# Kernel tuning notes

Hardware: AMD Instinct MI355X
Metric: run time of the kernel (lower is better)

Reference implementation:

```python
import jax, jax.numpy as jnp
import numpy as np

N_NODES = 100000


def _graph_conv(x, W, b, src, dst, n_nodes):
    # dgl GraphConv, norm='both'. in_dim >= out_dim so weight is applied first.
    E = src.shape[0]
    ones = jnp.ones((E,), dtype=x.dtype)
    deg_out = jnp.clip(jax.ops.segment_sum(ones, src, num_segments=n_nodes), 1.0)
    deg_in = jnp.clip(jax.ops.segment_sum(ones, dst, num_segments=n_nodes), 1.0)
    h = x @ W                                  # [N, out]
    h = h * (deg_out ** -0.5)[:, None]          # src-side norm D_out^{-1/2}
    agg = jax.ops.segment_sum(h[src], dst, num_segments=n_nodes)  # SpMM
    agg = agg * (deg_in ** -0.5)[:, None]       # dst-side norm D_in^{-1/2}
    return agg + b


def setup_inputs() -> dict:
    key = jax.random.key(0)
    k1, k2, k3, k4, k5, k6, k7 = jax.random.split(key, 7)
    in_dim, hidden_dim, out_dim = 256, 128, 40
    E = 3200000
    h = jax.random.normal(k1, (N_NODES, in_dim), dtype=jnp.float32)
    src = jax.random.randint(k2, (E,), 0, N_NODES)
    dst = jax.random.randint(k3, (E,), 0, N_NODES)
    # Glorot-style init for GraphConv weights, zero bias (dgl default)
    W1 = jax.random.normal(k4, (in_dim, hidden_dim), dtype=jnp.float32) / np.sqrt(in_dim)
    b1 = jnp.zeros((hidden_dim,), dtype=jnp.float32)
    W2 = jax.random.normal(k5, (hidden_dim, out_dim), dtype=jnp.float32) / np.sqrt(hidden_dim)
    b2 = jnp.zeros((out_dim,), dtype=jnp.float32)
    return {"h": h, "W1": W1, "b1": b1, "W2": W2, "b2": b2, "src": src, "dst": dst}


def reference(h, W1, b1, W2, b2, src, dst):
    n = h.shape[0]
    # CRD: GraphConv -> relu (dropout is identity in eval)
    x = _graph_conv(h, W1, b1, src, dst, n)
    x = jax.nn.relu(x)
    # CLS: GraphConv -> log_softmax over classes
    x = _graph_conv(x, W2, b2, src, dst, n)
    return jax.nn.log_softmax(x, axis=1)
```

## Files before the change

kernel.cpp:

```cpp
#include <hip/hip_runtime.h>
#include <hip/hip_bf16.h>
#include <cstddef>
#include <cstdint>

#define IN_DIM 256
#define HID 128
#define OUT_DIM 40

#define CHUNK 4096
#define BIN_SHIFT 10
#define BIN_SIZE 1024
#define MAXB 128
#define GSPLIT 8

typedef __attribute__((ext_vector_type(8))) short short8;
typedef __attribute__((ext_vector_type(4))) float f32x4;
typedef __attribute__((ext_vector_type(2))) float f32x2;

__device__ inline short f2bf(float f) {
    __hip_bfloat16 b = __float2bfloat16(f);
    return __builtin_bit_cast(short, b);
}
__device__ inline float bf2f(unsigned short u) {
    unsigned int v = (unsigned int)u << 16;
    return __builtin_bit_cast(float, v);
}
__device__ inline int permf(int p) { return (p >> 3) + 16 * (p & 7); }

__global__ __launch_bounds__(256) void k_init(const float* __restrict__ W1, const float* __restrict__ W2,
                                              const float* __restrict__ b1, short* __restrict__ Wg,
                                              short* __restrict__ Wg2, float* __restrict__ b1p,
                                              int* __restrict__ deg_in, int* __restrict__ deg_out, int Z,
                                              const int* __restrict__ src, const int* __restrict__ dst,
                                              uint32_t* __restrict__ stD, unsigned short* __restrict__ stS,
                                              int* __restrict__ bboD, int* __restrict__ bboS,
                                              int E, int NBINS, int setupBlocks) {
    __shared__ __align__(16) uint32_t sgD[CHUNK];
    __shared__ __align__(16) unsigned short sgS[CHUNK];
    __shared__ int hD[MAXB], hS[MAXB], sd[MAXB];
    int t = threadIdx.x;
    if (blockIdx.x < setupBlocks) {
        int flat = blockIdx.x * 256 + t;
        if (flat < 8192) {
            int k = flat >> 5;
            int n0 = (flat & 31) * 4;
            float4 v = *(const float4*)(W1 + (size_t)k * HID + n0);
            int ks = k >> 5, quad = (k >> 3) & 3, j = k & 7;
            float vv[4] = {v.x, v.y, v.z, v.w};
#pragma unroll
            for (int e = 0; e < 4; ++e) {
                int n = n0 + e;
                int nt = n >> 4;
                int ln = (n & 15) | (quad << 4);
                Wg[(((nt * 8 + ks) * 64) + ln) * 8 + j] = f2bf(vv[e]);
            }
            return;
        }
        flat -= 8192;
        if (flat < 3 * 4 * 64 * 8) {
            int f = flat >> 9;
            int ln = (flat >> 3) & 63;
            int j = flat & 7;
            int nt = f >> 2, ks = f & 3;
            int q = ks * 32 + (ln >> 4) * 8 + j;
            int c = nt * 16 + (ln & 15);
            float v = (c < OUT_DIM) ? W2[(size_t)permf(q) * OUT_DIM + c] : 0.f;
            Wg2[flat] = f2bf(v);
            return;
        }
        flat -= 3 * 4 * 64 * 8;
        if (flat < HID) { b1p[flat] = b1[permf(flat)]; return; }
        flat -= HID;
        if (flat < Z) { *(int4*)(deg_in + flat * 4) = make_int4(0, 0, 0, 0); return; }
        flat -= Z;
        if (flat < Z) { *(int4*)(deg_out + flat * 4) = make_int4(0, 0, 0, 0); }
        return;
    }
    int j = blockIdx.x - setupBlocks;
    int base = j * CHUNK;
    int nE = min(CHUNK, E - base);
    int NB1 = NBINS + 1;
    for (int i = t; i < MAXB; i += 256) { hD[i] = 0; hS[i] = 0; }
    __syncthreads();
    for (int i = t; i < nE; i += 256) {
        atomicAdd(&hD[dst[base + i] >> BIN_SHIFT], 1);
        atomicAdd(&hS[src[base + i] >> BIN_SHIFT], 1);
    }
    __syncthreads();
    if (t < MAXB) sd[t] = hD[t];
    __syncthreads();
    for (int off = 1; off < MAXB; off <<= 1) {
        int x = 0;
        if (t < MAXB && t >= off) x = sd[t - off];
        __syncthreads();
        if (t < MAXB) sd[t] += x;
        __syncthreads();
    }
    if (t < MAXB) {
        int h = hD[t];
        int c = sd[t] - h;
        hD[t] = c;
        if (t < NBINS) bboD[(size_t)j * NB1 + t] = c;
    }
    if (t == NBINS) bboD[(size_t)j * NB1 + NBINS] = nE;
    __syncthreads();
    if (t < MAXB) sd[t] = hS[t];
    __syncthreads();
    for (int off = 1; off < MAXB; off <<= 1) {
        int x = 0;
        if (t < MAXB && t >= off) x = sd[t - off];
        __syncthreads();
        if (t < MAXB) sd[t] += x;
        __syncthreads();
    }
    if (t < MAXB) {
        int h = hS[t];
        int c = sd[t] - h;
        hS[t] = c;
        if (t < NBINS) bboS[(size_t)j * NB1 + t] = c;
    }
    if (t == NBINS) bboS[(size_t)j * NB1 + NBINS] = nE;
    __syncthreads();
    for (int i = t; i < nE; i += 256) {
        int s = src[base + i], d = dst[base + i];
        int pD = atomicAdd(&hD[d >> BIN_SHIFT], 1);
        sgD[pD] = ((uint32_t)(d & (BIN_SIZE - 1)) << 17) | (uint32_t)s;
        int pS = atomicAdd(&hS[s >> BIN_SHIFT], 1);
        sgS[pS] = (unsigned short)(s & (BIN_SIZE - 1));
    }
    __syncthreads();
    int nh = nE >> 1;
    uint2* dD = (uint2*)(stD + base);
    const uint2* sD = (const uint2*)sgD;
    for (int i = t; i < nh; i += 256) dD[i] = sD[i];
    uint32_t* dS = (uint32_t*)(stS + base);
    const uint32_t* sS = (const uint32_t*)sgS;
    for (int i = t; i < nh; i += 256) dS[i] = sS[i];
    if ((nE & 1) && t == 0) { stD[base + nE - 1] = sgD[nE - 1]; stS[base + nE - 1] = sgS[nE - 1]; }
}

__global__ __launch_bounds__(256) void k_deg(const uint32_t* __restrict__ stD, const int* __restrict__ bboD,
                                             const unsigned short* __restrict__ stS, const int* __restrict__ bboS,
                                             int* __restrict__ deg_in, int* __restrict__ deg_out,
                                             int* __restrict__ hsave, int nchunk, int NBINS) {
    __shared__ int hist[BIN_SIZE];
    int b = blockIdx.x, g = blockIdx.y, t = threadIdx.x;
    int wv = t >> 6, lane = t & 63;
    int NB1 = NBINS + 1;
    for (int i = t; i < BIN_SIZE; i += 256) hist[i] = 0;
    __syncthreads();
    int base = b << BIN_SHIFT;
    if (blockIdx.z == 0) {
        for (int j = g * 4 + wv; j < nchunk; j += GSPLIT * 4) {
            int s = bboD[(size_t)j * NB1 + b], e = bboD[(size_t)j * NB1 + b + 1];
            const uint32_t* seg = stD + (size_t)j * CHUNK;
            for (int i = s + lane; i < e; i += 64)
                atomicAdd(&hist[seg[i] >> 17], 1);
        }
        __syncthreads();
        int* hp = hsave + ((size_t)(b * GSPLIT + g) << BIN_SHIFT);
        for (int i = t; i < BIN_SIZE; i += 256) {
            int v = hist[i];
            hp[i] = v;
            if (v) atomicAdd(&deg_in[base + i], v);
        }
    } else {
        for (int j = g * 4 + wv; j < nchunk; j += GSPLIT * 4) {
            int s = bboS[(size_t)j * NB1 + b], e = bboS[(size_t)j * NB1 + b + 1];
            const unsigned short* seg = stS + (size_t)j * CHUNK;
            for (int i = s + lane; i < e; i += 64)
                atomicAdd(&hist[seg[i]], 1);
        }
        __syncthreads();
        for (int i = t; i < BIN_SIZE; i += 256) {
            int v = hist[i];
            if (v) atomicAdd(&deg_out[base + i], v);
        }
    }
}

__global__ __launch_bounds__(256) void k_scan1(const int* __restrict__ deg, int* __restrict__ out,
                                               int* __restrict__ bsum, float* __restrict__ rs_in, int n) {
    __shared__ int sd[256];
    int t = threadIdx.x, b = blockIdx.x;
    int base = b * 1024 + t * 4;
    int v0 = 0, v1 = 0, v2 = 0, v3 = 0;
    if (base + 0 < n) v0 = deg[base + 0];
    if (base + 1 < n) v1 = deg[base + 1];
    if (base + 2 < n) v2 = deg[base + 2];
    if (base + 3 < n) v3 = deg[base + 3];
    if (base + 0 < n) rs_in[base + 0] = rsqrtf((float)max(v0, 1));
    if (base + 1 < n) rs_in[base + 1] = rsqrtf((float)max(v1, 1));
    if (base + 2 < n) rs_in[base + 2] = rsqrtf((float)max(v2, 1));
    if (base + 3 < n) rs_in[base + 3] = rsqrtf((float)max(v3, 1));
    int ts = v0 + v1 + v2 + v3;
    sd[t] = ts;
    __syncthreads();
    for (int off = 1; off < 256; off <<= 1) {
        int x = 0;
        if (t >= off) x = sd[t - off];
        __syncthreads();
        sd[t] += x;
        __syncthreads();
    }
    int excl = sd[t] - ts;
    if (base + 0 < n) out[base + 0] = excl;
    if (base + 1 < n) out[base + 1] = excl + v0;
    if (base + 2 < n) out[base + 2] = excl + v0 + v1;
    if (base + 3 < n) out[base + 3] = excl + v0 + v1 + v2;
    if (t == 255) bsum[b] = sd[255];
}

__global__ __launch_bounds__(256) void k_scan3(int* __restrict__ row_ptr, const int* __restrict__ bsum,
                                               int* __restrict__ cursor, const int* __restrict__ deg_out,
                                               float* __restrict__ rs_out, int n, int E, int NB) {
    __shared__ int sb[128];
    int t = threadIdx.x;
    if (t < 128) sb[t] = (t < NB) ? bsum[t] : 0;
    __syncthreads();
    for (int off = 1; off < 128; off <<= 1) {
        int x = 0;
        if (t < 128 && t >= off) x = sb[t - off];
        __syncthreads();
        if (t < 128) sb[t] += x;
        __syncthreads();
    }
    int i = blockIdx.x * 256 + threadIdx.x;
    if (i < n) {
        int blk = i >> 10;
        int add = (blk > 0) ? sb[blk - 1] : 0;
        int v = row_ptr[i] + add;
        row_ptr[i] = v;
        cursor[i] = v;
        rs_out[i] = rsqrtf((float)max(deg_out[i], 1));
    }
    if (i == 0) row_ptr[n] = E;
}

__global__ __launch_bounds__(256) void k_colgemm1(const uint32_t* __restrict__ stD, const int* __restrict__ bboD,
                                                  const int* __restrict__ hsave, int* __restrict__ cursor,
                                                  int* __restrict__ col, int nchunk, int NBINS, int colBlocks,
                                                  const float* __restrict__ A, const short* __restrict__ Wg,
                                                  const float* __restrict__ rs_out, uint32_t* __restrict__ h1f,
                                                  int M) {
    __shared__ int hist[BIN_SIZE];
    int t = threadIdx.x;
    if (blockIdx.x < colBlocks) {
        int b = blockIdx.x / GSPLIT, g = blockIdx.x % GSPLIT;
        int wv = t >> 6, lane = t & 63;
        int NB1 = NBINS + 1;
        int base = b << BIN_SHIFT;
        const int* hp = hsave + ((size_t)(b * GSPLIT + g) << BIN_SHIFT);
        for (int i = t; i < BIN_SIZE; i += 256) {
            int v = hp[i];
            hist[i] = v ? atomicAdd(&cursor[base + i], v) : 0;
        }
        __syncthreads();
        for (int j = g * 4 + wv; j < nchunk; j += GSPLIT * 4) {
            int s = bboD[(size_t)j * NB1 + b], e = bboD[(size_t)j * NB1 + b + 1];
            const uint32_t* seg = stD + (size_t)j * CHUNK;
            for (int i = s + lane; i < e; i += 64) {
                uint32_t v = seg[i];
                int pos = atomicAdd(&hist[v >> 17], 1);
                col[pos] = (int)(v & 0x1FFFFu);
            }
        }
        return;
    }
    int lane = t & 63, wv = t >> 6;
    int block_row = (blockIdx.x - colBlocks) * 64;
    int row = block_row + wv * 16 + (lane & 15);
    bool valid = row < M;
    const float* ap = A + (size_t)row * IN_DIM + (lane >> 4) * 8;
    f32x4 acc[8] = {};
#pragma unroll
    for (int ks = 0; ks < 8; ++ks) {
        float4 va = {0.f, 0.f, 0.f, 0.f}, vb = {0.f, 0.f, 0.f, 0.f};
        if (valid) {
            va = *(const float4*)(ap + ks * 32);
            vb = *(const float4*)(ap + ks * 32 + 4);
        }
        short8 a;
        a[0] = f2bf(va.x); a[1] = f2bf(va.y); a[2] = f2bf(va.z); a[3] = f2bf(va.w);
        a[4] = f2bf(vb.x); a[5] = f2bf(vb.y); a[6] = f2bf(vb.z); a[7] = f2bf(vb.w);
#pragma unroll
        for (int nt = 0; nt < 8; ++nt) {
            short8 b = *(const short8*)&Wg[(((nt * 8 + ks) * 64) + lane) * 8];
            acc[nt] = __builtin_amdgcn_mfma_f32_16x16x32_bf16(a, b, acc[nt], 0, 0, 0);
        }
    }
    int quad = lane >> 4, cl = lane & 15;
#pragma unroll
    for (int r = 0; r < 4; ++r) {
        int gr = block_row + wv * 16 + quad * 4 + r;
        if (gr >= M) continue;
        float sc = rs_out[gr];
        int d0 = __builtin_amdgcn_cvt_pk_fp8_f32(acc[0][r] * sc, acc[1][r] * sc, 0, false);
        d0 = __builtin_amdgcn_cvt_pk_fp8_f32(acc[2][r] * sc, acc[3][r] * sc, d0, true);
        int d1 = __builtin_amdgcn_cvt_pk_fp8_f32(acc[4][r] * sc, acc[5][r] * sc, 0, false);
        d1 = __builtin_amdgcn_cvt_pk_fp8_f32(acc[6][r] * sc, acc[7][r] * sc, d1, true);
        uint2 dd = make_uint2((uint32_t)d0, (uint32_t)d1);
        *(uint2*)((char*)h1f + (size_t)gr * 128 + cl * 8) = dd;
    }
}

__global__ __launch_bounds__(256) void k_spmm1f(const char* __restrict__ h1c, const int* __restrict__ rp,
                                                const int* __restrict__ col, const float* __restrict__ rs_in,
                                                const float* __restrict__ rs_out, const float* __restrict__ b1p,
                                                const short* __restrict__ Wg2,
                                                uint32_t* __restrict__ h2f, int N) {
    __shared__ uint32_t x1s[16 * 64];
    __shared__ uint32_t hs2[48];
    int t = threadIdx.x;
    int wv = t >> 6, lane = t & 63;
    int grp = lane >> 4, ql = lane & 15;
    int w_base = blockIdx.x * 4;
    int w = w_base + wv;

    float4 blo = *(const float4*)&b1p[ql * 8];
    float4 bhi = *(const float4*)&b1p[ql * 8 + 4];

    if (w < N) {
        int s = rp[w], e = rp[w + 1];
        f32x2 a0 = {0.f, 0.f}, a1 = {0.f, 0.f}, a2 = {0.f, 0.f}, a3 = {0.f, 0.f};
        int qoff = ql << 3;
        int i = s;
        while (i < e) {
            int cnt = min(64, e - i);
            int cl = (lane < cnt) ? lane : cnt - 1;
            int rof = col[i + cl] << 7;
            int nfull = cnt & ~15;
            int it = 0;
            for (; it < nfull; it += 16) {
                int o0 = __shfl(rof, it + grp, 64) + qoff;
                int o1 = __shfl(rof, it + 4 + grp, 64) + qoff;
                int o2 = __shfl(rof, it + 8 + grp, 64) + qoff;
                int o3 = __shfl(rof, it + 12 + grp, 64) + qoff;
                uint2 u0 = *(const uint2*)(h1c + (uint32_t)o0);
                uint2 u1 = *(const uint2*)(h1c + (uint32_t)o1);
                uint2 u2 = *(const uint2*)(h1c + (uint32_t)o2);
                uint2 u3 = *(const uint2*)(h1c + (uint32_t)o3);
                a0 += __builtin_amdgcn_cvt_pk_f32_fp8(u0.x, false);
                a1 += __builtin_amdgcn_cvt_pk_f32_fp8(u0.x, true);
                a2 += __builtin_amdgcn_cvt_pk_f32_fp8(u0.y, false);
                a3 += __builtin_amdgcn_cvt_pk_f32_fp8(u0.y, true);
                a0 += __builtin_amdgcn_cvt_pk_f32_fp8(u1.x, false);
                a1 += __builtin_amdgcn_cvt_pk_f32_fp8(u1.x, true);
                a2 += __builtin_amdgcn_cvt_pk_f32_fp8(u1.y, false);
                a3 += __builtin_amdgcn_cvt_pk_f32_fp8(u1.y, true);
                a0 += __builtin_amdgcn_cvt_pk_f32_fp8(u2.x, false);
                a1 += __builtin_amdgcn_cvt_pk_f32_fp8(u2.x, true);
                a2 += __builtin_amdgcn_cvt_pk_f32_fp8(u2.y, false);
                a3 += __builtin_amdgcn_cvt_pk_f32_fp8(u2.y, true);
                a0 += __builtin_amdgcn_cvt_pk_f32_fp8(u3.x, false);
                a1 += __builtin_amdgcn_cvt_pk_f32_fp8(u3.x, true);
                a2 += __builtin_amdgcn_cvt_pk_f32_fp8(u3.y, false);
                a3 += __builtin_amdgcn_cvt_pk_f32_fp8(u3.y, true);
            }
            if (it < cnt) {
                int e0 = it + grp;
                int o0 = __shfl(rof, e0, 64) + qoff;
                int o1 = __shfl(rof, e0 + 4, 64) + qoff;
                int o2 = __shfl(rof, e0 + 8, 64) + qoff;
                int o3 = __shfl(rof, e0 + 12, 64) + qoff;
                float mv0 = (e0 < cnt) ? 1.f : 0.f;
                float mv1 = (e0 + 4 < cnt) ? 1.f : 0.f;
                float mv2 = (e0 + 8 < cnt) ? 1.f : 0.f;
                float mv3 = (e0 + 12 < cnt) ? 1.f : 0.f;
                f32x2 m0 = {mv0, mv0}, m1 = {mv1, mv1}, m2 = {mv2, mv2}, m3 = {mv3, mv3};
                uint2 u0 = *(const uint2*)(h1c + (uint32_t)o0);
                uint2 u1 = *(const uint2*)(h1c + (uint32_t)o1);
                uint2 u2 = *(const uint2*)(h1c + (uint32_t)o2);
                uint2 u3 = *(const uint2*)(h1c + (uint32_t)o3);
                a0 += __builtin_amdgcn_cvt_pk_f32_fp8(u0.x, false) * m0;
                a1 += __builtin_amdgcn_cvt_pk_f32_fp8(u0.x, true) * m0;
                a2 += __builtin_amdgcn_cvt_pk_f32_fp8(u0.y, false) * m0;
                a3 += __builtin_amdgcn_cvt_pk_f32_fp8(u0.y, true) * m0;
                a0 += __builtin_amdgcn_cvt_pk_f32_fp8(u1.x, false) * m1;
                a1 += __builtin_amdgcn_cvt_pk_f32_fp8(u1.x, true) * m1;
                a2 += __builtin_amdgcn_cvt_pk_f32_fp8(u1.y, false) * m1;
                a3 += __builtin_amdgcn_cvt_pk_f32_fp8(u1.y, true) * m1;
                a0 += __builtin_amdgcn_cvt_pk_f32_fp8(u2.x, false) * m2;
                a1 += __builtin_amdgcn_cvt_pk_f32_fp8(u2.x, true) * m2;
                a2 += __builtin_amdgcn_cvt_pk_f32_fp8(u2.y, false) * m2;
                a3 += __builtin_amdgcn_cvt_pk_f32_fp8(u2.y, true) * m2;
                a0 += __builtin_amdgcn_cvt_pk_f32_fp8(u3.x, false) * m3;
                a1 += __builtin_amdgcn_cvt_pk_f32_fp8(u3.x, true) * m3;
                a2 += __builtin_amdgcn_cvt_pk_f32_fp8(u3.y, false) * m3;
                a3 += __builtin_amdgcn_cvt_pk_f32_fp8(u3.y, true) * m3;
            }
            i += cnt;
        }
        float ac[8] = {a0.x, a0.y, a1.x, a1.y, a2.x, a2.y, a3.x, a3.y};
#pragma unroll
        for (int j = 0; j < 8; ++j) {
            ac[j] += __shfl_xor(ac[j], 16, 64);
            ac[j] += __shfl_xor(ac[j], 32, 64);
        }
        if (lane < 16) {
            float sc = rs_in[w];
            float f0, f1;
            uint32_t o0, o1, o2, o3;
            f0 = fmaxf(fmaf(ac[0], sc, blo.x), 0.f); f1 = fmaxf(fmaf(ac[1], sc, blo.y), 0.f);
            o0 = (uint32_t)(unsigned short)f2bf(f0) | ((uint32_t)(unsigned short)f2bf(f1) << 16);
            f0 = fmaxf(fmaf(ac[2], sc, blo.z), 0.f); f1 = fmaxf(fmaf(ac[3], sc, blo.w), 0.f);
            o1 = (uint32_t)(unsigned short)f2bf(f0) | ((uint32_t)(unsigned short)f2bf(f1) << 16);
            f0 = fmaxf(fmaf(ac[4], sc, bhi.x), 0.f); f1 = fmaxf(fmaf(ac[5], sc, bhi.y), 0.f);
            o2 = (uint32_t)(unsigned short)f2bf(f0) | ((uint32_t)(unsigned short)f2bf(f1) << 16);
            f0 = fmaxf(fmaf(ac[6], sc, bhi.z), 0.f); f1 = fmaxf(fmaf(ac[7], sc, bhi.w), 0.f);
            o3 = (uint32_t)(unsigned short)f2bf(f0) | ((uint32_t)(unsigned short)f2bf(f1) << 16);
            int woff = (wv * 256 + ql * 16) ^ ((wv & 7) << 4);
            *(uint4*)((char*)x1s + woff) = make_uint4(o0, o1, o2, o3);
        }
    }
    __syncthreads();
    int vr = min(4, N - w_base);
    if (wv < 3) {
        short8 wf0 = *(const short8*)&Wg2[((wv * 4 + 0) * 64 + lane) * 8];
        short8 wf1 = *(const short8*)&Wg2[((wv * 4 + 1) * 64 + lane) * 8];
        short8 wf2 = *(const short8*)&Wg2[((wv * 4 + 2) * 64 + lane) * 8];
        short8 wf3 = *(const short8*)&Wg2[((wv * 4 + 3) * 64 + lane) * 8];
        int row = lane & 15, kc = lane >> 4;
        int rbase = row * 256 + kc * 16;
        int swz = (row & 7) << 4;
        f32x4 c = {};
        c = __builtin_amdgcn_mfma_f32_16x16x32_bf16(*(short8*)((char*)x1s + ((rbase + 0) ^ swz)),   wf0, c, 0, 0, 0);
        c = __builtin_amdgcn_mfma_f32_16x16x32_bf16(*(short8*)((char*)x1s + ((rbase + 64) ^ swz)),  wf1, c, 0, 0, 0);
        c = __builtin_amdgcn_mfma_f32_16x16x32_bf16(*(short8*)((char*)x1s + ((rbase + 128) ^ swz)), wf2, c, 0, 0, 0);
        c = __builtin_amdgcn_mfma_f32_16x16x32_bf16(*(short8*)((char*)x1s + ((rbase + 192) ^ swz)), wf3, c, 0, 0, 0);
        int cc = wv * 16 + row;
        if (cc < OUT_DIM && kc == 0) {
            float s0 = rs_out[w_base + 0];
            float s1 = (vr > 1) ? rs_out[w_base + 1] : 0.f;
            float s2 = (vr > 2) ? rs_out[w_base + 2] : 0.f;
            float s3 = (vr > 3) ? rs_out[w_base + 3] : 0.f;
            int pk = __builtin_amdgcn_cvt_pk_fp8_f32(c[0] * s0, c[1] * s1, 0, false);
            pk = __builtin_amdgcn_cvt_pk_fp8_f32(c[2] * s2, c[3] * s3, pk, true);
            hs2[cc] = (uint32_t)pk;
        }
    }
    __syncthreads();
    if (t < 64) {
        int node = t >> 4, d = t & 15;
        uint32_t v = 0;
        if (d < 10) {
            int sh = node * 8;
            uint32_t b0 = (hs2[4 * d + 0] >> sh) & 0xffu;
            uint32_t b1 = (hs2[4 * d + 1] >> sh) & 0xffu;
            uint32_t b2 = (hs2[4 * d + 2] >> sh) & 0xffu;
            uint32_t b3 = (hs2[4 * d + 3] >> sh) & 0xffu;
            v = b0 | (b1 << 8) | (b2 << 16) | (b3 << 24);
        }
        if (node < vr) h2f[(size_t)(w_base + node) * 16 + d] = v;
    }
}

__global__ __launch_bounds__(256) void k_spmm2(const char* __restrict__ h2c, const int* __restrict__ rp,
                                               const int* __restrict__ col, const float* __restrict__ rs_in,
                                               const float* __restrict__ b2, float* __restrict__ out, int n) {
    int w = (blockIdx.x * 256 + threadIdx.x) >> 6;
    int lane = threadIdx.x & 63;
    if (w >= n) return;
    int grp = lane >> 3, fl = lane & 7;
    int qoff = fl << 3;
    int s = rp[w], e = rp[w + 1];
    f32x2 a0 = {0.f, 0.f}, a1 = {0.f, 0.f}, a2 = {0.f, 0.f}, a3 = {0.f, 0.f};
    int i = s;
    while (i < e) {
        int cnt = min(64, e - i);
        int cl = (lane < cnt) ? lane : cnt - 1;
        int rof = col[i + cl] << 6;
        int nfull = cnt & ~31;
        int it = 0;
        for (; it < nfull; it += 32) {
            int o0 = __shfl(rof, it + grp, 64) + qoff;
            int o1 = __shfl(rof, it + 8 + grp, 64) + qoff;
            int o2 = __shfl(rof, it + 16 + grp, 64) + qoff;
            int o3 = __shfl(rof, it + 24 + grp, 64) + qoff;
            uint2 u0 = *(const uint2*)(h2c + (uint32_t)o0);
            uint2 u1 = *(const uint2*)(h2c + (uint32_t)o1);
            uint2 u2 = *(const uint2*)(h2c + (uint32_t)o2);
            uint2 u3 = *(const uint2*)(h2c + (uint32_t)o3);
            a0 += __builtin_amdgcn_cvt_pk_f32_fp8(u0.x, false);
            a1 += __builtin_amdgcn_cvt_pk_f32_fp8(u0.x, true);
            a2 += __builtin_amdgcn_cvt_pk_f32_fp8(u0.y, false);
            a3 += __builtin_amdgcn_cvt_pk_f32_fp8(u0.y, true);
            a0 += __builtin_amdgcn_cvt_pk_f32_fp8(u1.x, false);
            a1 += __builtin_amdgcn_cvt_pk_f32_fp8(u1.x, true);
            a2 += __builtin_amdgcn_cvt_pk_f32_fp8(u1.y, false);
            a3 += __builtin_amdgcn_cvt_pk_f32_fp8(u1.y, true);
            a0 += __builtin_amdgcn_cvt_pk_f32_fp8(u2.x, false);
            a1 += __builtin_amdgcn_cvt_pk_f32_fp8(u2.x, true);
            a2 += __builtin_amdgcn_cvt_pk_f32_fp8(u2.y, false);
            a3 += __builtin_amdgcn_cvt_pk_f32_fp8(u2.y, true);
            a0 += __builtin_amdgcn_cvt_pk_f32_fp8(u3.x, false);
            a1 += __builtin_amdgcn_cvt_pk_f32_fp8(u3.x, true);
            a2 += __builtin_amdgcn_cvt_pk_f32_fp8(u3.y, false);
            a3 += __builtin_amdgcn_cvt_pk_f32_fp8(u3.y, true);
        }
        if (it < cnt) {
            int e0 = it + grp;
            int o0 = __shfl(rof, e0, 64) + qoff;
            int o1 = __shfl(rof, e0 + 8, 64) + qoff;
            int o2 = __shfl(rof, e0 + 16, 64) + qoff;
            int o3 = __shfl(rof, e0 + 24, 64) + qoff;
            float mv0 = (e0 < cnt) ? 1.f : 0.f;
            float mv1 = (e0 + 8 < cnt) ? 1.f : 0.f;
            float mv2 = (e0 + 16 < cnt) ? 1.f : 0.f;
            float mv3 = (e0 + 24 < cnt) ? 1.f : 0.f;
            f32x2 m0 = {mv0, mv0}, m1 = {mv1, mv1}, m2 = {mv2, mv2}, m3 = {mv3, mv3};
            uint2 u0 = *(const uint2*)(h2c + (uint32_t)o0);
            uint2 u1 = *(const uint2*)(h2c + (uint32_t)o1);
            uint2 u2 = *(const uint2*)(h2c + (uint32_t)o2);
            uint2 u3 = *(const uint2*)(h2c + (uint32_t)o3);
            a0 += __builtin_amdgcn_cvt_pk_f32_fp8(u0.x, false) * m0;
            a1 += __builtin_amdgcn_cvt_pk_f32_fp8(u0.x, true) * m0;
            a2 += __builtin_amdgcn_cvt_pk_f32_fp8(u0.y, false) * m0;
            a3 += __builtin_amdgcn_cvt_pk_f32_fp8(u0.y, true) * m0;
            a0 += __builtin_amdgcn_cvt_pk_f32_fp8(u1.x, false) * m1;
            a1 += __builtin_amdgcn_cvt_pk_f32_fp8(u1.x, true) * m1;
            a2 += __builtin_amdgcn_cvt_pk_f32_fp8(u1.y, false) * m1;
            a3 += __builtin_amdgcn_cvt_pk_f32_fp8(u1.y, true) * m1;
            a0 += __builtin_amdgcn_cvt_pk_f32_fp8(u2.x, false) * m2;
            a1 += __builtin_amdgcn_cvt_pk_f32_fp8(u2.x, true) * m2;
            a2 += __builtin_amdgcn_cvt_pk_f32_fp8(u2.y, false) * m2;
            a3 += __builtin_amdgcn_cvt_pk_f32_fp8(u2.y, true) * m2;
            a0 += __builtin_amdgcn_cvt_pk_f32_fp8(u3.x, false) * m3;
            a1 += __builtin_amdgcn_cvt_pk_f32_fp8(u3.x, true) * m3;
            a2 += __builtin_amdgcn_cvt_pk_f32_fp8(u3.y, false) * m3;
            a3 += __builtin_amdgcn_cvt_pk_f32_fp8(u3.y, true) * m3;
        }
        i += cnt;
    }
    float ac[8] = {a0.x, a0.y, a1.x, a1.y, a2.x, a2.y, a3.x, a3.y};
#pragma unroll
    for (int j = 0; j < 8; ++j) {
        ac[j] += __shfl_xor(ac[j], 8, 64);
        ac[j] += __shfl_xor(ac[j], 16, 64);
        ac[j] += __shfl_xor(ac[j], 32, 64);
    }
    bool act = lane < 5;
    float sc = rs_in[w];
    int bb = (fl < 5) ? fl * 8 : 0;
    float val[8];
#pragma unroll
    for (int j = 0; j < 8; ++j)
        val[j] = fmaf(ac[j], sc, b2[bb + j]);
    float pm = -INFINITY;
    if (act) {
        pm = val[0];
#pragma unroll
        for (int j = 1; j < 8; ++j) pm = fmaxf(pm, val[j]);
    }
    pm = fmaxf(pm, __shfl_xor(pm, 4, 8));
    pm = fmaxf(pm, __shfl_xor(pm, 2, 8));
    pm = fmaxf(pm, __shfl_xor(pm, 1, 8));
    float ex = 0.f;
    if (act) {
#pragma unroll
        for (int j = 0; j < 8; ++j) ex += expf(val[j] - pm);
    }
    ex += __shfl_xor(ex, 4, 8);
    ex += __shfl_xor(ex, 2, 8);
    ex += __shfl_xor(ex, 1, 8);
    if (act) {
        float l = pm + logf(ex);
        float4 o0 = {val[0] - l, val[1] - l, val[2] - l, val[3] - l};
        float4 o1 = {val[4] - l, val[5] - l, val[6] - l, val[7] - l};
        float* op = out + (size_t)w * OUT_DIM + lane * 8;
        *(float4*)op = o0;
        *(float4*)(op + 4) = o1;
    }
}


extern "C" void kernel_launch(void* const* d_in, const int* in_sizes, int n_in,
                              void* d_out, int out_size, void* d_ws, size_t ws_size,
                              hipStream_t stream) {
    const int N = in_sizes[0] / IN_DIM;
    const int E = in_sizes[5];
    const float* h  = (const float*)d_in[0];
    const float* W1 = (const float*)d_in[1];
    const float* b1 = (const float*)d_in[2];
    const float* W2 = (const float*)d_in[3];
    const float* b2 = (const float*)d_in[4];
    const int* src  = (const int*)d_in[5];
    const int* dst  = (const int*)d_in[6];
    float* out = (float*)d_out;

    const int NBINS  = (N + BIN_SIZE - 1) >> BIN_SHIFT;
    const int NCHUNK = (E + CHUNK - 1) / CHUNK;

    char* w = (char*)d_ws;
    size_t off = 0;
    auto alloc = [&](size_t bytes) -> void* {
        void* p = w + off;
        off += (bytes + 255) & ~(size_t)255;
        return p;
    };
    int* deg_in   = (int*)alloc((size_t)N * 4);
    int* deg_out  = (int*)alloc((size_t)N * 4);
    int* row_ptr  = (int*)alloc((size_t)(N + 1) * 4);
    int* cursor   = (int*)alloc((size_t)N * 4);
    int* bsum     = (int*)alloc(1024 * 4);
    float* rs_out = (float*)alloc((size_t)N * 4);
    float* rs_in  = (float*)alloc((size_t)N * 4);
    int* col      = (int*)alloc((size_t)E * 4);
    int* bboD     = (int*)alloc((size_t)NCHUNK * (NBINS + 1) * 4);
    int* bboS     = (int*)alloc((size_t)NCHUNK * (NBINS + 1) * 4);
    short* Wg     = (short*)alloc((size_t)8 * 8 * 64 * 8 * 2);
    short* Wg2    = (short*)alloc((size_t)3 * 4 * 64 * 8 * 2);
    float* b1p    = (float*)alloc((size_t)HID * 4);
    int* hsave    = (int*)alloc((size_t)NBINS * GSPLIT * BIN_SIZE * 4);
    uint32_t* stD = (uint32_t*)alloc((size_t)E * 4);
    unsigned short* stS = (unsigned short*)alloc((size_t)E * 2);
    uint32_t* h1f = (uint32_t*)alloc((size_t)N * HID);
    uint32_t* h2f = (uint32_t*)alloc((size_t)N * 64);

    int gN = (N + 255) / 256;
    int NB = (N + 1023) / 1024;
    int Z = (N + 3) / 4;
    int setup_units = 8192 + 3 * 4 * 64 * 8 + HID + 2 * Z;
    int setupBlocks = (setup_units + 255) / 256;
    int colBlocks = NBINS * GSPLIT;

    k_init<<<setupBlocks + NCHUNK, 256, 0, stream>>>(W1, W2, b1, Wg, Wg2, b1p, deg_in, deg_out, Z,
                                                     src, dst, stD, stS, bboD, bboS, E, NBINS, setupBlocks);
    k_deg<<<dim3(NBINS, GSPLIT, 2), 256, 0, stream>>>(stD, bboD, stS, bboS, deg_in, deg_out, hsave, NCHUNK, NBINS);
    k_scan1<<<NB, 256, 0, stream>>>(deg_in, row_ptr, bsum, rs_in, N);
    k_scan3<<<gN, 256, 0, stream>>>(row_ptr, bsum, cursor, deg_out, rs_out, N, E, NB);
    k_colgemm1<<<colBlocks + (N + 63) / 64, 256, 0, stream>>>(stD, bboD, hsave, cursor, col, NCHUNK, NBINS,
                                                              colBlocks, h, Wg, rs_out, h1f, N);
    k_spmm1f<<<(N + 3) / 4, 256, 0, stream>>>((const char*)h1f, row_ptr, col, rs_in, rs_out, b1p, Wg2, h2f, N);
    k_spmm2<<<(N + 3) / 4, 256, 0, stream>>>((const char*)h2f, row_ptr, col, rs_in, b2, out, N);
}
```

Before: 416.4 us.

## Scatter CSR columns with one block per bin, dropping per-split histogram save

The column-scatter phase now uses a single block per 1024-node bin that seeds its shared-memory cursors straight from row_ptr. This removes the hsave per-split histogram buffer, the global cursor array and the global atomics that reserved offsets per split. The chunk loop also batches four chunks' bounds and first loads before the atomics to expose memory-level parallelism. In exchange, only about 98 blocks do the scatter instead of roughly 784, so each block serially walks every chunk. That may leave the scatter starved of parallelism unless it overlaps well with the GEMM blocks in the same launch.

After: 459.9 us. +10.5%, slower.

```diff
diff --git a/kernel.cpp b/kernel.cpp
--- a/kernel.cpp
+++ b/kernel.cpp
@@ -142,7 +142,7 @@
 __global__ __launch_bounds__(256) void k_deg(const uint32_t* __restrict__ stD, const int* __restrict__ bboD,
                                              const unsigned short* __restrict__ stS, const int* __restrict__ bboS,
                                              int* __restrict__ deg_in, int* __restrict__ deg_out,
-                                             int* __restrict__ hsave, int nchunk, int NBINS) {
+                                             int nchunk, int NBINS) {
     __shared__ int hist[BIN_SIZE];
     int b = blockIdx.x, g = blockIdx.y, t = threadIdx.x;
     int wv = t >> 6, lane = t & 63;
@@ -158,10 +158,8 @@
                 atomicAdd(&hist[seg[i] >> 17], 1);
         }
         __syncthreads();
-        int* hp = hsave + ((size_t)(b * GSPLIT + g) << BIN_SHIFT);
         for (int i = t; i < BIN_SIZE; i += 256) {
             int v = hist[i];
-            hp[i] = v;
             if (v) atomicAdd(&deg_in[base + i], v);
         }
     } else {
@@ -212,7 +210,7 @@
 }
 
 __global__ __launch_bounds__(256) void k_scan3(int* __restrict__ row_ptr, const int* __restrict__ bsum,
-                                               int* __restrict__ cursor, const int* __restrict__ deg_out,
+                                               const int* __restrict__ deg_out,
                                                float* __restrict__ rs_out, int n, int E, int NB) {
     __shared__ int sb[128];
     int t = threadIdx.x;
@@ -229,46 +227,66 @@
     if (i < n) {
         int blk = i >> 10;
         int add = (blk > 0) ? sb[blk - 1] : 0;
-        int v = row_ptr[i] + add;
-        row_ptr[i] = v;
-        cursor[i] = v;
+        row_ptr[i] += add;
         rs_out[i] = rsqrtf((float)max(deg_out[i], 1));
     }
     if (i == 0) row_ptr[n] = E;
 }
 
 __global__ __launch_bounds__(256) void k_colgemm1(const uint32_t* __restrict__ stD, const int* __restrict__ bboD,
-                                                  const int* __restrict__ hsave, int* __restrict__ cursor,
-                                                  int* __restrict__ col, int nchunk, int NBINS, int colBlocks,
+                                                  const int* __restrict__ row_ptr, int* __restrict__ col,
+                                                  int nchunk, int NBINS,
                                                   const float* __restrict__ A, const short* __restrict__ Wg,
                                                   const float* __restrict__ rs_out, uint32_t* __restrict__ h1f,
                                                   int M) {
-    __shared__ int hist[BIN_SIZE];
+    __shared__ int cur[BIN_SIZE];
     int t = threadIdx.x;
-    if (blockIdx.x < colBlocks) {
-        int b = blockIdx.x / GSPLIT, g = blockIdx.x % GSPLIT;
+    if (blockIdx.x < (unsigned)NBINS) {
+        int b = blockIdx.x;
         int wv = t >> 6, lane = t & 63;
         int NB1 = NBINS + 1;
         int base = b << BIN_SHIFT;
-        const int* hp = hsave + ((size_t)(b * GSPLIT + g) << BIN_SHIFT);
         for (int i = t; i < BIN_SIZE; i += 256) {
-            int v = hp[i];
-            hist[i] = v ? atomicAdd(&cursor[base + i], v) : 0;
-        }
-        __syncthreads();
-        for (int j = g * 4 + wv; j < nchunk; j += GSPLIT * 4) {
-            int s = bboD[(size_t)j * NB1 + b], e = bboD[(size_t)j * NB1 + b + 1];
-            const uint32_t* seg = stD + (size_t)j * CHUNK;
-            for (int i = s + lane; i < e; i += 64) {
-                uint32_t v = seg[i];
-                int pos = atomicAdd(&hist[v >> 17], 1);
-                col[pos] = (int)(v & 0x1FFFFu);
+            int gn = base + i;
+            cur[i] = (gn < M) ? row_ptr[gn] : 0;
+        }
+        __syncthreads();
+        for (int jj = wv * 4; jj < nchunk; jj += 16) {
+            int s[4], e[4];
+            uint32_t v[4];
+            bool av[4];
+#pragma unroll
+            for (int q = 0; q < 4; ++q) {
+                int j = jj + q;
+                bool jv = j < nchunk;
+                s[q] = jv ? bboD[(size_t)j * NB1 + b] : 0;
+                e[q] = jv ? bboD[(size_t)j * NB1 + b + 1] : 0;
             }
+#pragma unroll
+            for (int q = 0; q < 4; ++q) {
+                av[q] = s[q] + lane < e[q];
+                v[q] = av[q] ? stD[(size_t)(jj + q) * CHUNK + s[q] + lane] : 0u;
+            }
+#pragma unroll
+            for (int q = 0; q < 4; ++q) {
+                if (av[q]) {
+                    int pos = atomicAdd(&cur[v[q] >> 17], 1);
+                    col[pos] = (int)(v[q] & 0x1FFFFu);
+                }
+            }
+#pragma unroll
+            for (int q = 0; q < 4; ++q) {
+                for (int i = s[q] + lane + 64; i < e[q]; i += 64) {
+                    uint32_t vv = stD[(size_t)(jj + q) * CHUNK + i];
+                    int pos = atomicAdd(&cur[vv >> 17], 1);
+                    col[pos] = (int)(vv & 0x1FFFFu);
+                }
+            }
         }
         return;
     }
     int lane = t & 63, wv = t >> 6;
-    int block_row = (blockIdx.x - colBlocks) * 64;
+    int block_row = (blockIdx.x - NBINS) * 64;
     int row = block_row + wv * 16 + (lane & 15);
     bool valid = row < M;
     const float* ap = A + (size_t)row * IN_DIM + (lane >> 4) * 8;
@@ -601,7 +619,6 @@
     int* deg_in   = (int*)alloc((size_t)N * 4);
     int* deg_out  = (int*)alloc((size_t)N * 4);
     int* row_ptr  = (int*)alloc((size_t)(N + 1) * 4);
-    int* cursor   = (int*)alloc((size_t)N * 4);
     int* bsum     = (int*)alloc(1024 * 4);
     float* rs_out = (float*)alloc((size_t)N * 4);
     float* rs_in  = (float*)alloc((size_t)N * 4);
@@ -611,7 +628,6 @@
     short* Wg     = (short*)alloc((size_t)8 * 8 * 64 * 8 * 2);
     short* Wg2    = (short*)alloc((size_t)3 * 4 * 64 * 8 * 2);
     float* b1p    = (float*)alloc((size_t)HID * 4);
-    int* hsave    = (int*)alloc((size_t)NBINS * GSPLIT * BIN_SIZE * 4);
     uint32_t* stD = (uint32_t*)alloc((size_t)E * 4);
     unsigned short* stS = (unsigned short*)alloc((size_t)E * 2);
     uint32_t* h1f = (uint32_t*)alloc((size_t)N * HID);
@@ -622,15 +638,14 @@
     int Z = (N + 3) / 4;
     int setup_units = 8192 + 3 * 4 * 64 * 8 + HID + 2 * Z;
     int setupBlocks = (setup_units + 255) / 256;
-    int colBlocks = NBINS * GSPLIT;
 
     k_init<<<setupBlocks + NCHUNK, 256, 0, stream>>>(W1, W2, b1, Wg, Wg2, b1p, deg_in, deg_out, Z,
                                                      src, dst, stD, stS, bboD, bboS, E, NBINS, setupBlocks);
-    k_deg<<<dim3(NBINS, GSPLIT, 2), 256, 0, stream>>>(stD, bboD, stS, bboS, deg_in, deg_out, hsave, NCHUNK, NBINS);
+    k_deg<<<dim3(NBINS, GSPLIT, 2), 256, 0, stream>>>(stD, bboD, stS, bboS, deg_in, deg_out, NCHUNK, NBINS);
     k_scan1<<<NB, 256, 0, stream>>>(deg_in, row_ptr, bsum, rs_in, N);
-    k_scan3<<<gN, 256, 0, stream>>>(row_ptr, bsum, cursor, deg_out, rs_out, N, E, NB);
-    k_colgemm1<<<colBlocks + (N + 63) / 64, 256, 0, stream>>>(stD, bboD, hsave, cursor, col, NCHUNK, NBINS,
-                                                              colBlocks, h, Wg, rs_out, h1f, N);
+    k_scan3<<<gN, 256, 0, stream>>>(row_ptr, bsum, deg_out, rs_out, N, E, NB);
+    k_colgemm1<<<NBINS + (N + 63) / 64, 256, 0, stream>>>(stD, bboD, row_ptr, col, NCHUNK, NBINS,
+                                                          h, Wg, rs_out, h1f, N);
     k_spmm1f<<<(N + 3) / 4, 256, 0, stream>>>((const char*)h1f, row_ptr, col, rs_in, rs_out, b1p, Wg2, h2f, N);
     k_spmm2<<<(N + 3) / 4, 256, 0, stream>>>((const char*)h2f, row_ptr, col, rs_in, b2, out, N);
 }
```
